# Kernel optimization log

Hardware: AMD Instinct MI355X
Metric: run time of the kernel (lower is better)

The kernel has to match this reference:

```python
import jax, jax.numpy as jnp
import numpy as np

N, CIN, T, V = 32, 64, 256, 25
COUT = 192
K = 3                      # num_subset
INTER = COUT // 4          # coff_embedding = 4 -> 48
MID = COUT // 3            # 64
EPS = 1e-5


def _bn(x, g, b):
    # training-mode BatchNorm2d over (N, T, V) per channel
    m = x.mean(axis=(0, 2, 3), keepdims=True)
    v = x.var(axis=(0, 2, 3), keepdims=True)
    return (x - m) * jax.lax.rsqrt(v + EPS) * g[None, :, None, None] + b[None, :, None, None]


def _conv1x1(x, w, b):
    # w: [O, C]
    return jnp.einsum('oc,nctv->notv', w, x) + b[None, :, None, None]


def _tconv(x, w, b, pad):
    # w: [O, C, k, 1] temporal conv along T
    y = jax.lax.conv_general_dilated(x, w, (1, 1), ((pad, pad), (0, 0)),
                                     dimension_numbers=('NCHW', 'OIHW', 'NCHW'))
    return y + b[None, :, None, None]


def setup_inputs() -> dict:
    key = jax.random.key(0)
    ks = jax.random.split(key, 24)
    r = lambda i, shape, s=0.05: jax.random.normal(ks[i], shape, jnp.float32) * s
    return {
        'x': r(0, (N, CIN, T, V), 1.0),
        'A': jax.random.uniform(ks[1], (K, V, V), jnp.float32),   # fixed adjacency buffer
        'PA': jnp.full((K, V, V), 1e-6, jnp.float32),
        'Wa': r(2, (K, INTER, CIN)), 'ba': jnp.zeros((K, INTER), jnp.float32),
        'Wb': r(3, (K, INTER, CIN)), 'bb': jnp.zeros((K, INTER), jnp.float32),
        'Wd': r(4, (K, COUT, CIN)), 'bd': jnp.zeros((K, COUT), jnp.float32),
        'gcn_bn_g': jnp.ones(COUT, jnp.float32), 'gcn_bn_b': jnp.zeros(COUT, jnp.float32),
        'down_w': r(5, (COUT, CIN)), 'down_b': jnp.zeros(COUT, jnp.float32),
        'down_bn_g': jnp.ones(COUT, jnp.float32), 'down_bn_b': jnp.zeros(COUT, jnp.float32),
        'W11': r(6, (COUT, COUT)), 'b11': jnp.zeros(COUT, jnp.float32),
        'W21': r(7, (COUT, COUT)), 'b21': jnp.zeros(COUT, jnp.float32),
        'W31': r(8, (COUT, COUT)), 'b31': jnp.zeros(COUT, jnp.float32),
        'W12': r(9, (MID, COUT, 1, 1)), 'b12': jnp.zeros(MID, jnp.float32),
        'W22': r(10, (MID, COUT, 3, 1)), 'b22': jnp.zeros(MID, jnp.float32),
        'W32': r(11, (MID, COUT, 7, 1)), 'b32': jnp.zeros(MID, jnp.float32),
        'tcn_bn_g': jnp.ones(COUT, jnp.float32), 'tcn_bn_b': jnp.zeros(COUT, jnp.float32),
        'res_w': r(12, (COUT, CIN)), 'res_b': jnp.zeros(COUT, jnp.float32),
        'res_bn_g': jnp.ones(COUT, jnp.float32), 'res_bn_b': jnp.zeros(COUT, jnp.float32),
    }


def reference(x, A, PA, Wa, ba, Wb, bb, Wd, bd, gcn_bn_g, gcn_bn_b,
              down_w, down_b, down_bn_g, down_bn_b,
              W11, b11, W21, b21, W31, b31, W12, b12, W22, b22, W32, b32,
              tcn_bn_g, tcn_bn_b, res_w, res_b, res_bn_g, res_bn_b):
    n, c, t, v = x.shape
    # ---- unit_gcn (all num_subset branches vectorized over axis k) ----
    fa = jnp.einsum('kic,nctv->nkitv', Wa, x) + ba[None, :, :, None, None]
    fb = jnp.einsum('kic,nctv->nkitv', Wb, x) + bb[None, :, :, None, None]
    A1 = fa.transpose(0, 1, 4, 2, 3).reshape(n, K, v, INTER * t)   # [n,k,V,inter*T]
    A2 = fb.reshape(n, K, INTER * t, v)                            # [n,k,inter*T,V]
    scores = jnp.einsum('nkvd,nkdw->nkvw', A1, A2) / A1.shape[-1]
    att = jax.nn.softmax(scores, axis=-2) + (A + PA)[None]         # softmax over rows (dim -2)
    xv = x.reshape(n, c * t, v)
    z = jnp.einsum('ndv,nkvw->nkdw', xv, att).reshape(n, K, c, t, v)
    y = jnp.einsum('koc,nkctv->notv', Wd, z) + bd.sum(axis=0)[None, :, None, None]
    y = _bn(y, gcn_bn_g, gcn_bn_b)
    y = y + _bn(_conv1x1(x, down_w, down_b), down_bn_g, down_bn_b)
    g = jax.nn.relu(y)
    # ---- unit_tcn_m: three parallel (1x1 conv -> temporal conv) branches ----
    x1 = _tconv(_conv1x1(g, W11, b11), W12, b12, 0)
    x2 = _tconv(_conv1x1(g, W21, b21), W22, b22, 1)
    x3 = _tconv(_conv1x1(g, W31, b31), W32, b32, 3)
    tm = _bn(jnp.concatenate([x1, x2, x3], axis=1), tcn_bn_g, tcn_bn_b)
    # ---- residual: 1x1 unit_tcn on original input ----
    res = _bn(_conv1x1(x, res_w, res_b), res_bn_g, res_bn_b)
    return jax.nn.relu(tm + res)
```

## Files before the change

kernel.cpp:

```cpp
#include <hip/hip_runtime.h>
#include <hip/hip_bf16.h>
#include <cstdint>
#include <cstddef>

#define EPS_  1e-5f
#define NTV_  204800

typedef unsigned short u16;
typedef __attribute__((ext_vector_type(8))) short short8;
typedef __attribute__((ext_vector_type(4))) float f32x4;

__device__ __forceinline__ float bf2f(u16 u) {
  uint32_t x = (uint32_t)u << 16;
  float f;
  __builtin_memcpy(&f, &x, 4);
  return f;
}
__device__ __forceinline__ u16 f2bf(float f) {
  uint32_t x;
  __builtin_memcpy(&x, &f, 4);
  uint32_t r = (x + 0x7FFFu + ((x >> 16) & 1u)) >> 16;
  return (u16)r;
}

__device__ __forceinline__ void gload_lds16(const u16* g, u16* l) {
  __builtin_amdgcn_global_load_lds(
      (const __attribute__((address_space(1))) uint32_t*)g,
      (__attribute__((address_space(3))) uint32_t*)l, 16, 0, 0);
}

__global__ __launch_bounds__(256) void k_cvtw(
    const float* __restrict__ Wa, const float* __restrict__ Wb_,
    const float* __restrict__ dw, const float* __restrict__ rw,
    const float* __restrict__ W11, const float* __restrict__ W21, const float* __restrict__ W31,
    const float* __restrict__ Wd, const float* __restrict__ W12, const float* __restrict__ W22,
    const float* __restrict__ W32, const float* __restrict__ bd,
    const float* __restrict__ ba, const float* __restrict__ bb,
    const float* __restrict__ downbi, const float* __restrict__ resbi,
    const float* __restrict__ b11, const float* __restrict__ b21, const float* __restrict__ b31,
    u16* __restrict__ WB, float* __restrict__ bd2, float* __restrict__ fbias,
    float* __restrict__ cbias)
{
  int i = blockIdx.x * 256 + threadIdx.x;
  if (i < 9216) { WB[i] = f2bf(Wa[i]); return; }
  i -= 9216;
  if (i < 9216) { WB[9216 + i] = f2bf(Wb_[i]); return; }
  i -= 9216;
  if (i < 12288) { WB[18432 + i] = f2bf(dw[i]); return; }
  i -= 12288;
  if (i < 12288) { WB[30720 + i] = f2bf(rw[i]); return; }
  i -= 12288;
  if (i < 36864) { WB[43008 + i] = f2bf(W11[i]); return; }
  i -= 36864;
  if (i < 36864) { WB[79872 + i] = f2bf(W21[i]); return; }
  i -= 36864;
  if (i < 36864) { WB[116736 + i] = f2bf(W31[i]); return; }
  i -= 36864;
  if (i < 36864) {
    const int o = i / 192, r = i % 192, k = r >> 6, c = r & 63;
    WB[153600 + i] = f2bf(Wd[((size_t)(k * 192 + o)) * 64 + c]);
    return;
  }
  i -= 36864;
  if (i < 12288) { WB[190464 + i] = f2bf(W12[i]); return; }
  i -= 12288;
  if (i < 36864) {
    const int tap = i / 12288, q = i % 12288, o = q / 192, c = q % 192;
    WB[202752 + i] = f2bf(W22[((size_t)(o * 192 + c)) * 3 + tap]);
    return;
  }
  i -= 36864;
  if (i < 86016) {
    const int tap = i / 12288, q = i % 12288, o = q / 192, c = q % 192;
    WB[239616 + i] = f2bf(W32[((size_t)(o * 192 + c)) * 7 + tap]);
    return;
  }
  i -= 86016;
  if (i < 192) { bd2[i] = bd[i] + bd[192 + i] + bd[384 + i]; return; }
  i -= 192;
  if (i < 288) { fbias[i] = (i < 144) ? ba[i] : bb[i - 144]; return; }
  i -= 288;
  if (i < 960) {
    const int g = i / 192, o = i % 192;
    float v;
    if (g == 0) v = downbi[o];
    else if (g == 1) v = resbi[o];
    else if (g == 2) v = b11[o];
    else if (g == 3) v = b21[o];
    else v = b31[o];
    cbias[i] = v;
  }
}

__global__ __launch_bounds__(256) void k_xpose(const float* __restrict__ x, u16* __restrict__ xb)
{
  __shared__ u16 xt[256][72];
  const int bx = blockIdx.x;
  const int n = bx / 25, s0 = (bx % 25) * 256;
  const int tid = threadIdx.x;
  for (int l = tid; l < 64 * 64; l += 256) {
    const int c = l >> 6, q = l & 63;
    float4 v = *(const float4*)&x[((size_t)n * 64 + c) * 6400 + s0 + q * 4];
    xt[q * 4 + 0][c] = f2bf(v.x);
    xt[q * 4 + 1][c] = f2bf(v.y);
    xt[q * 4 + 2][c] = f2bf(v.z);
    xt[q * 4 + 3][c] = f2bf(v.w);
  }
  __syncthreads();
  for (int l = tid; l < 256 * 8; l += 256) {
    const int row = l >> 3, seg = l & 7;
    const int s_old = s0 + row;
    const int dv = s_old % 25, dt = s_old / 25;
    *(uint4*)&xb[((size_t)n * 6400 + dv * 256 + dt) * 64 + seg * 8] = *(const uint4*)&xt[row][seg * 8];
  }
}

template<int C, int NP, bool STATS>
__global__ __launch_bounds__(192) void k_conv5(
    const u16* __restrict__ in, const u16* __restrict__ Wb,
    const float* __restrict__ bias,
    u16* __restrict__ out0, u16* __restrict__ out1, u16* __restrict__ out2,
    float* __restrict__ stSum, float* __restrict__ stSq)
{
  constexpr int CS = C / 8;
  constexpr int CH = C / 32;
  constexpr int SB = 128 * CS;
  __shared__ u16 Bt[128 * C];
  __shared__ u16 Ep[3][16 * 72];

  const int bx = blockIdx.x;
  const int nb = bx / 50;
  const int sb = (bx % 50) * 128;
  const int tid = threadIdx.x;
  const int w = tid >> 6, lane = tid & 63;
  const int lr = lane & 15, lg = lane >> 4;

  for (int base = 0; base < SB; base += 192) {
    const int slot = base + tid;
    if ((SB % 192 == 0) || slot < SB) {
      const int r = slot / CS, q = slot % CS;
      gload_lds16(&in[((size_t)nb * 6400 + sb + r) * C + ((q ^ (r & 7)) << 3)],
                  &Bt[(size_t)(base + w * 64) * 8]);
    }
  }
  __syncthreads();

  u16* sc = Ep[w];
  const int o_w = w * 64;
  const int s0 = lane >> 3, seg = lane & 7;

  for (int p = 0; p < NP; ++p) {
    u16* outp = (p == 0) ? out0 : ((p == 1) ? out1 : out2);
    const u16* Ap = Wb + (size_t)p * 192 * C;
    short8 af[4][CH];
#pragma unroll
    for (int mi = 0; mi < 4; ++mi)
#pragma unroll
      for (int j = 0; j < CH; ++j)
        af[mi][j] = *(const short8*)&Ap[((size_t)(o_w + mi * 16 + lr)) * C + j * 32 + lg * 8];
    float4 bv[4];
#pragma unroll
    for (int mi = 0; mi < 4; ++mi)
      bv[mi] = *(const float4*)&bias[p * 192 + o_w + mi * 16 + lg * 4];
    float ssum[4][4] = {}, ssq[4][4] = {};

#pragma unroll
    for (int t = 0; t < 8; ++t) {
      f32x4 acc[4];
#pragma unroll
      for (int mi = 0; mi < 4; ++mi) {
        acc[mi][0] = 0.f; acc[mi][1] = 0.f; acc[mi][2] = 0.f; acc[mi][3] = 0.f;
      }
      const int rr = t * 16 + lr;
#pragma unroll
      for (int j = 0; j < CH; ++j) {
        short8 bf = *(const short8*)&Bt[((size_t)rr * CS + ((j * 4 + lg) ^ (rr & 7))) * 8];
#pragma unroll
        for (int mi = 0; mi < 4; ++mi)
          acc[mi] = __builtin_amdgcn_mfma_f32_16x16x32_bf16(af[mi][j], bf, acc[mi], 0, 0, 0);
      }
#pragma unroll
      for (int mi = 0; mi < 4; ++mi)
#pragma unroll
        for (int r = 0; r < 4; ++r) {
          float vv = acc[mi][r] + ((const float*)&bv[mi])[r];
          if (STATS) { ssum[mi][r] += vv; ssq[mi][r] += vv * vv; }
          sc[lr * 72 + mi * 16 + lg * 4 + r] = f2bf(vv);
        }
#pragma unroll
      for (int pass = 0; pass < 2; ++pass) {
        const int s = pass * 8 + s0;
        uint4 val = *(const uint4*)&sc[s * 72 + seg * 8];
        *(uint4*)&outp[((size_t)nb * 6400 + sb + t * 16 + s) * 192 + o_w + seg * 8] = val;
      }
    }

    if (STATS) {
#pragma unroll
      for (int mi = 0; mi < 4; ++mi)
#pragma unroll
        for (int r = 0; r < 4; ++r) {
          float ss = ssum[mi][r], sq = ssq[mi][r];
#pragma unroll
          for (int m = 1; m < 16; m <<= 1) { ss += __shfl_xor(ss, m); sq += __shfl_xor(sq, m); }
          if (lr == 0) {
            const int og = p * 192 + o_w + mi * 16 + lg * 4 + r;
            const int slot = bx & 15;
            atomicAdd(&stSum[og * 16 + slot], ss);
            atomicAdd(&stSq[og * 16 + slot], sq);
          }
        }
    }
  }
}

__global__ __launch_bounds__(256) void k_tconv7(
    const u16* __restrict__ b1, const u16* __restrict__ b2, const u16* __restrict__ b3,
    const u16* __restrict__ WB,
    const float* __restrict__ bias12, const float* __restrict__ bias22, const float* __restrict__ bias32,
    u16* __restrict__ out, float* __restrict__ stSum, float* __restrict__ stSq,
    const u16* __restrict__ zp)
{
  constexpr int C = 192, CS = 24, CH = 6;
  constexpr int BR = 70;
  __shared__ u16 Bt[BR * C];
  __shared__ u16 Ep[64][200];

  const int bx = blockIdx.x;
  const int nb = bx / 100;
  const int sb = (bx % 100) * 64;
  const int tbase = sb & 255;
  const int tid = threadIdx.x;
  const int w = tid >> 6, lane = tid & 63;
  const int lr = lane & 15, lg = lane >> 4;

  for (int br = 0; br < 3; ++br) {
    const u16* in = (br == 0) ? b1 : ((br == 1) ? b2 : b3);
    const float* bias = (br == 0) ? bias12 : ((br == 1) ? bias22 : bias32);
    const int KT = (br == 0) ? 1 : ((br == 1) ? 3 : 7);
    const u16* Wp = WB + ((br == 0) ? 190464 : ((br == 1) ? 202752 : 239616));

    if (br) __syncthreads();
    constexpr int SB = BR * CS;
    for (int base = 0; base < SB; base += 256) {
      const int slot = base + tid;
      if (slot < SB) {
        const int r = slot / CS, q = slot % CS;
        const int t = tbase - 3 + r;
        const u16* src = ((unsigned)t < 256u)
            ? &in[((size_t)nb * 6400 + sb - 3 + r) * C + ((q ^ (r & 7)) << 3)]
            : zp;
        gload_lds16(src, &Bt[(size_t)(base + w * 64) * 8]);
      }
    }
    __syncthreads();

    f32x4 acc[4];
#pragma unroll
    for (int t = 0; t < 4; ++t) {
      acc[t][0] = 0.f; acc[t][1] = 0.f; acc[t][2] = 0.f; acc[t][3] = 0.f;
    }
    const int hofs = 3 - KT / 2;
    for (int tap = 0; tap < KT; ++tap) {
      short8 af[CH];
#pragma unroll
      for (int j = 0; j < CH; ++j)
        af[j] = *(const short8*)&Wp[((size_t)(tap * 64 + w * 16 + lr)) * C + j * 32 + lg * 8];
#pragma unroll
      for (int t = 0; t < 4; ++t) {
        const int rr = t * 16 + lr + hofs + tap;
#pragma unroll
        for (int j = 0; j < CH; ++j) {
          short8 bf = *(const short8*)&Bt[((size_t)rr * CS + ((j * 4 + lg) ^ (rr & 7))) * 8];
          acc[t] = __builtin_amdgcn_mfma_f32_16x16x32_bf16(af[j], bf, acc[t], 0, 0, 0);
        }
      }
    }

    const float4 bv4 = *(const float4*)&bias[w * 16 + lg * 4];
    float ssum[4] = {}, ssq[4] = {};
#pragma unroll
    for (int t = 0; t < 4; ++t) {
      union { uint2 u; u16 s[4]; } pk;
#pragma unroll
      for (int r = 0; r < 4; ++r) {
        float vv = acc[t][r] + ((const float*)&bv4)[r];
        ssum[r] += vv; ssq[r] += vv * vv;
        pk.s[r] = f2bf(vv);
      }
      *(uint2*)&Ep[t * 16 + lr][br * 64 + w * 16 + lg * 4] = pk.u;
    }
#pragma unroll
    for (int r = 0; r < 4; ++r) {
      float ss = ssum[r], sq = ssq[r];
#pragma unroll
      for (int m = 1; m < 16; m <<= 1) { ss += __shfl_xor(ss, m); sq += __shfl_xor(sq, m); }
      if (lr == 0) {
        const int og = br * 64 + w * 16 + lg * 4 + r;
        const int slot = bx & 15;
        atomicAdd(&stSum[og * 16 + slot], ss);
        atomicAdd(&stSq[og * 16 + slot], sq);
      }
    }
  }
  __syncthreads();

#pragma unroll
  for (int pass = 0; pass < 6; ++pass) {
    const int idx = pass * 256 + tid;
    const int row = idx / 24, ch = idx % 24;
    *(uint4*)&out[((size_t)nb * 6400 + sb + row) * 192 + ch * 8] = *(const uint4*)&Ep[row][ch * 8];
  }
}

__global__ __launch_bounds__(256) void k_gemm_cf(
    const u16* __restrict__ in, const u16* __restrict__ Wb,
    const float* __restrict__ bias, u16* __restrict__ out)
{
  __shared__ u16 Bt[128 * 64];
  __shared__ u16 At[288 * 64];
  __shared__ u16 SC[48 * 136];

  const int bx = blockIdx.x;
  const int nb = bx / 50;
  const int sb = (bx % 50) * 128;
  const int v = sb >> 8, tbase = sb & 255;
  const int tid = threadIdx.x;
  const int w = tid >> 6, lane = tid & 63;
  const int lr = lane & 15, lg = lane >> 4;
  const int s_w = w * 32;

  for (int base = 0; base < 1024; base += 256) {
    const int slot = base + tid;
    const int r = slot >> 3, q = slot & 7;
    gload_lds16(&in[((size_t)nb * 6400 + v * 256 + tbase + r) * 64 + ((q ^ (r & 7)) << 3)],
                &Bt[(size_t)(base + w * 64) * 8]);
  }
  for (int base = 0; base < 2304; base += 256) {
    const int slot = base + tid;
    const int r = slot >> 3, q = slot & 7;
    gload_lds16(&Wb[(size_t)r * 64 + ((q ^ (r & 7)) << 3)],
                &At[(size_t)(base + w * 64) * 8]);
  }
  __syncthreads();

  for (int p = 0; p < 6; ++p) {
    f32x4 acc[3][2];
#pragma unroll
    for (int mi = 0; mi < 3; ++mi)
#pragma unroll
      for (int ni = 0; ni < 2; ++ni) {
        acc[mi][ni][0] = 0.f; acc[mi][ni][1] = 0.f; acc[mi][ni][2] = 0.f; acc[mi][ni][3] = 0.f;
      }
#pragma unroll
    for (int ch = 0; ch < 2; ++ch) {
      const int j = ch * 4 + lg;
      short8 af[3], bf[2];
#pragma unroll
      for (int mi = 0; mi < 3; ++mi) {
        const int r = p * 48 + mi * 16 + lr;
        af[mi] = *(const short8*)&At[((size_t)r * 8 + (j ^ (r & 7))) * 8];
      }
#pragma unroll
      for (int ni = 0; ni < 2; ++ni) {
        const int r = s_w + ni * 16 + lr;
        bf[ni] = *(const short8*)&Bt[((size_t)r * 8 + (j ^ (r & 7))) * 8];
      }
#pragma unroll
      for (int mi = 0; mi < 3; ++mi)
#pragma unroll
        for (int ni = 0; ni < 2; ++ni)
          acc[mi][ni] = __builtin_amdgcn_mfma_f32_16x16x32_bf16(af[mi], bf[ni], acc[mi][ni], 0, 0, 0);
    }
#pragma unroll
    for (int mi = 0; mi < 3; ++mi)
#pragma unroll
      for (int r = 0; r < 4; ++r) {
        const float bv = bias[p * 48 + mi * 16 + lg * 4 + r];
#pragma unroll
        for (int ni = 0; ni < 2; ++ni) acc[mi][ni][r] += bv;
      }
    __syncthreads();
#pragma unroll
    for (int mi = 0; mi < 3; ++mi)
#pragma unroll
      for (int ni = 0; ni < 2; ++ni)
#pragma unroll
        for (int r = 0; r < 4; ++r)
          SC[(mi * 16 + lg * 4 + r) * 136 + s_w + ni * 16 + lr] = f2bf(acc[mi][ni][r]);
    __syncthreads();
#pragma unroll
    for (int it = 0; it < 3; ++it) {
      const int row = it * 16 + (tid >> 4), chunk = tid & 15;
      *(uint4*)&out[((size_t)nb * 288 + p * 48 + row) * 6400 + sb + chunk * 8] =
          *(const uint4*)&SC[row * 136 + chunk * 8];
    }
  }
}

__device__ __forceinline__ float dot4(uint2 a, uint2 b) {
  return bf2f((u16)(a.x & 0xffff)) * bf2f((u16)(b.x & 0xffff)) +
         bf2f((u16)(a.x >> 16))    * bf2f((u16)(b.x >> 16)) +
         bf2f((u16)(a.y & 0xffff)) * bf2f((u16)(b.y & 0xffff)) +
         bf2f((u16)(a.y >> 16))    * bf2f((u16)(b.y >> 16));
}

__global__ __launch_bounds__(256) void k_scores_part(
    const u16* __restrict__ fab, float* __restrict__ part)
{
  const int nk = blockIdx.x;
  const int seg = blockIdx.y;
  const int n = nk / 3, k = nk % 3;
  __shared__ u16 sa[12800], sb[12800];
  const int tid = threadIdx.x;
  const u16* fap = fab + ((size_t)(n * 288 + k * 48 + seg * 2)) * 6400;
  const u16* fbp = fab + ((size_t)(n * 288 + 144 + k * 48 + seg * 2)) * 6400;
  for (int l = tid; l < 1600; l += 256) {
    ((uint4*)sa)[l] = ((const uint4*)fap)[l];
    ((uint4*)sb)[l] = ((const uint4*)fbp)[l];
  }
  __syncthreads();

  const int l0 = tid, l1 = tid + 256, l2 = tid + 512;
  const bool ok2 = (l2 < 625);
  const int v0 = l0 / 25, w0 = l0 % 25;
  const int v1 = l1 / 25, w1 = l1 % 25;
  const int v2 = ok2 ? l2 / 25 : 0, w2 = ok2 ? l2 % 25 : 0;
  float a0 = 0.f, a1 = 0.f, a2 = 0.f;
  const int rot = ((tid & 63) * 4) & 255;

#pragma unroll
  for (int ch = 0; ch < 2; ++ch) {
    const u16* pa = sa + ch * 6400;
    const u16* pb = sb + ch * 6400;
    for (int it = 0; it < 64; ++it) {
      const int t = (it * 4 + rot) & 255;
      a0 += dot4(*(const uint2*)&pa[v0 * 256 + t], *(const uint2*)&pb[w0 * 256 + t]);
      a1 += dot4(*(const uint2*)&pa[v1 * 256 + t], *(const uint2*)&pb[w1 * 256 + t]);
      if (ok2)
        a2 += dot4(*(const uint2*)&pa[v2 * 256 + t], *(const uint2*)&pb[w2 * 256 + t]);
    }
  }
  float* po = part + ((size_t)nk * 24 + seg) * 640;
  po[l0] = a0;
  po[l1] = a1;
  if (ok2) po[l2] = a2;
}

__global__ __launch_bounds__(256) void k_softmax(
    const float* __restrict__ part, const float* __restrict__ A,
    const float* __restrict__ PA, float* __restrict__ att)
{
  const int nk = blockIdx.x;
  const int n = nk / 3, k = nk % 3;
  __shared__ float sc[640];
  const int tid = threadIdx.x;
  const float* pb = part + (size_t)nk * 24 * 640;
  for (int l = tid; l < 625; l += 256) {
    float s = 0.f;
#pragma unroll
    for (int seg = 0; seg < 24; ++seg) s += pb[seg * 640 + l];
    sc[l] = s;
  }
  __syncthreads();
  if (tid < 25) {
    const int w = tid;
    const float scale = 1.f / 12288.f;
    float m = -1e30f;
    for (int v = 0; v < 25; ++v) m = fmaxf(m, sc[v * 25 + w]);
    m *= scale;
    float e[25], sum = 0.f;
#pragma unroll
    for (int v = 0; v < 25; ++v) { e[v] = __expf(sc[v * 25 + w] * scale - m); sum += e[v]; }
    const float inv = 1.f / sum;
    const float* Ak = A + k * 625;
    const float* Pk = PA + k * 625;
    float* ao = att + ((size_t)n * 3 + k) * 625;
#pragma unroll
    for (int v = 0; v < 25; ++v) ao[v * 25 + w] = e[v] * inv + Ak[v * 25 + w] + Pk[v * 25 + w];
  }
}

__global__ __launch_bounds__(256) void k_z(
    const u16* __restrict__ xb, const float* __restrict__ att, u16* __restrict__ z)
{
  __shared__ float attl[1950];
  __shared__ u16 xt[12800];
  const int bx = blockIdx.x;
  const int n = bx >> 5, tb = (bx & 31) * 8;
  const int tid = threadIdx.x;

  for (int l = tid; l < 1875; l += 256) {
    const int k = l / 625, vw = l % 625, v = vw / 25, w = vw % 25;
    attl[(k * 25 + v) * 26 + w] = att[((size_t)n * 3 + k) * 625 + vw];
  }
  for (int l = tid; l < 200 * 8; l += 256) {
    const int j = l >> 3, seg = l & 7;
    const int vv = j >> 3, tl = j & 7;
    *(uint4*)&xt[j * 64 + seg * 8] =
        *(const uint4*)&xb[((size_t)n * 6400 + vv * 256 + tb + tl) * 64 + seg * 8];
  }
  __syncthreads();

  for (int it = 0; it < 19; ++it) {
    const int l = tid + it * 256;
    if (l >= 4800) break;
    const int hi = l >> 6, lo = l & 63;
    const int k = hi / 25, w = hi % 25;
    const int tl = lo >> 3, c0 = (lo & 7) * 8;
    float accv[8] = {};
    for (int v = 0; v < 25; ++v) {
      const float aw = attl[(k * 25 + v) * 26 + w];
      union { uint4 u; u16 s[8]; } xv;
      xv.u = *(const uint4*)&xt[(v * 8 + tl) * 64 + c0];
#pragma unroll
      for (int jj = 0; jj < 8; ++jj) accv[jj] += aw * bf2f(xv.s[jj]);
    }
    union { uint4 u; u16 s[8]; } ov;
#pragma unroll
    for (int jj = 0; jj < 8; ++jj) ov.s[jj] = f2bf(accv[jj]);
    *(uint4*)&z[((size_t)n * 6400 + w * 256 + tb + tl) * 192 + k * 64 + c0] = ov.u;
  }
}

__global__ void k_bnparams(const float* __restrict__ sSum, const float* __restrict__ sSq,
                           const float* __restrict__ gamma, const float* __restrict__ beta,
                           float* __restrict__ a, float* __restrict__ c, int O)
{
  const int o = threadIdx.x + blockIdx.x * blockDim.x;
  if (o >= O) return;
  float sum = 0.f, sq = 0.f;
#pragma unroll
  for (int s = 0; s < 16; ++s) { sum += sSum[o * 16 + s]; sq += sSq[o * 16 + s]; }
  const float mean = sum * (1.f / NTV_);
  const float var = sq * (1.f / NTV_) - mean * mean;
  const float inv = rsqrtf(var + EPS_);
  const float av = gamma[o] * inv;
  a[o] = av;
  c[o] = beta[o] - av * mean;
}

__global__ __launch_bounds__(256) void k_g2(
    const u16* __restrict__ ypre, const u16* __restrict__ down,
    const float* __restrict__ ga, const float* __restrict__ gc,
    const float* __restrict__ da, const float* __restrict__ dc,
    u16* __restrict__ g)
{
  __shared__ float pA1[192], pC1[192], pA2[192], pC2[192];
  const int tid = threadIdx.x;
  if (tid < 192) { pA1[tid] = ga[tid]; pC1[tid] = gc[tid]; pA2[tid] = da[tid]; pC2[tid] = dc[tid]; }
  __syncthreads();
  for (size_t i8 = (size_t)blockIdx.x * 256 + tid; i8 < 4915200; i8 += (size_t)gridDim.x * 256) {
    const int c0 = (int)(i8 % 24) * 8;
    union { uint4 u; u16 s[8]; } yv, dv, ov;
    yv.u = *(const uint4*)&ypre[i8 * 8];
    dv.u = *(const uint4*)&down[i8 * 8];
#pragma unroll
    for (int j = 0; j < 8; ++j) {
      const int c = c0 + j;
      ov.s[j] = f2bf(fmaxf(pA1[c] * bf2f(yv.s[j]) + pC1[c] + pA2[c] * bf2f(dv.s[j]) + pC2[c], 0.f));
    }
    *(uint4*)&g[i8 * 8] = ov.u;
  }
}

__global__ __launch_bounds__(256) void k_out(
    const u16* __restrict__ tm, const u16* __restrict__ resp,
    const float* __restrict__ ta, const float* __restrict__ tc,
    const float* __restrict__ ra, const float* __restrict__ rc,
    float* __restrict__ out)
{
  __shared__ u16 L[100][200];
  __shared__ float pA1[192], pC1[192], pA2[192], pC2[192];
  const int bx = blockIdx.x;
  const int n = bx >> 6, t0 = (bx & 63) * 4;
  const int tid = threadIdx.x;
  if (tid < 192) { pA1[tid] = ta[tid]; pC1[tid] = tc[tid]; pA2[tid] = ra[tid]; pC2[tid] = rc[tid]; }
  __syncthreads();
  for (int l = tid; l < 2400; l += 256) {
    const int row = l / 24, ch = l % 24;
    const int v = row >> 2, tl = row & 3;
    const size_t src = ((size_t)n * 6400 + v * 256 + t0 + tl) * 192 + ch * 8;
    union { uint4 u; u16 s[8]; } tv, rv;
    tv.u = *(const uint4*)&tm[src];
    rv.u = *(const uint4*)&resp[src];
#pragma unroll
    for (int j = 0; j < 8; ++j) {
      const int c = ch * 8 + j;
      L[row][c] = f2bf(fmaxf(pA1[c] * bf2f(tv.s[j]) + pC1[c] + pA2[c] * bf2f(rv.s[j]) + pC2[c], 0.f));
    }
  }
  __syncthreads();
  for (int j = tid; j < 192 * 25; j += 256) {
    const int o = j / 25, q = j % 25;
    float4 f4;
#pragma unroll
    for (int e = 0; e < 4; ++e) {
      const int idx = q * 4 + e;
      const int tl = idx / 25, v = idx % 25;
      ((float*)&f4)[e] = bf2f(L[v * 4 + tl][o]);
    }
    *(float4*)&out[((size_t)n * 192 + o) * 6400 + t0 * 25 + q * 4] = f4;
  }
}

extern "C" void kernel_launch(void* const* d_in, const int* in_sizes, int n_in,
                              void* d_out, int out_size, void* d_ws, size_t ws_size,
                              hipStream_t stream)
{
  const float* x      = (const float*)d_in[0];
  const float* A      = (const float*)d_in[1];
  const float* PA     = (const float*)d_in[2];
  const float* Wa     = (const float*)d_in[3];
  const float* ba     = (const float*)d_in[4];
  const float* Wb     = (const float*)d_in[5];
  const float* bb     = (const float*)d_in[6];
  const float* Wd     = (const float*)d_in[7];
  const float* bd     = (const float*)d_in[8];
  const float* gcng   = (const float*)d_in[9];
  const float* gcnb   = (const float*)d_in[10];
  const float* downw  = (const float*)d_in[11];
  const float* downbi = (const float*)d_in[12];
  const float* downg  = (const float*)d_in[13];
  const float* downb  = (const float*)d_in[14];
  const float* W11    = (const float*)d_in[15];
  const float* b11    = (const float*)d_in[16];
  const float* W21    = (const float*)d_in[17];
  const float* b21    = (const float*)d_in[18];
  const float* W31    = (const float*)d_in[19];
  const float* b31    = (const float*)d_in[20];
  const float* W12    = (const float*)d_in[21];
  const float* b12    = (const float*)d_in[22];
  const float* W22    = (const float*)d_in[23];
  const float* b22    = (const float*)d_in[24];
  const float* W32    = (const float*)d_in[25];
  const float* b32    = (const float*)d_in[26];
  const float* tcng   = (const float*)d_in[27];
  const float* tcnb   = (const float*)d_in[28];
  const float* resw   = (const float*)d_in[29];
  const float* resbi  = (const float*)d_in[30];
  const float* resg   = (const float*)d_in[31];
  const float* resb   = (const float*)d_in[32];
  (void)in_sizes; (void)n_in; (void)out_size; (void)ws_size;

  u16* ob = (u16*)d_out;
  u16* fab   = ob;
  u16* xb    = ob + 58982400;
  float* att = (float*)(ob + 72089600);
  float* part  = (float*)(ob + 72584768);
  float* fbias = (float*)(ob + 75533888);
  u16* btmp2 = ob;
  u16* btmp3 = ob + 39321600;

  char* ws = (char*)d_ws;
  const size_t SLOT = 78643200;
  u16* z     = (u16*)(ws);
  u16* g     = (u16*)(ws);
  u16* ypre  = (u16*)(ws + SLOT);
  u16* btmp1 = (u16*)(ws + SLOT);
  u16* down  = (u16*)(ws + 2 * SLOT);
  u16* tm    = (u16*)(ws + 2 * SLOT);
  u16* resp  = (u16*)(ws + 3 * SLOT);
  char* sm   = ws + 4 * SLOT;
  float* bnp   = (float*)(sm);
  u16*   zp    = (u16*)(sm + 8192);
  u16*   WB    = (u16*)(sm + 8704);
  float* bd2   = (float*)(sm + 660224);
  float* cbias = (float*)(sm + 661248);
  float* slots = (float*)(sm + 665600);
  float* gcnSum = slots;           float* gcnSq = slots + 3072;
  float* dwnSum = slots + 6144;    float* resSum = slots + 9216;
  float* dwnSq  = slots + 12288;   float* resSq  = slots + 15360;
  float* tmSum  = slots + 18432;   float* tmSq   = slots + 21504;
  float* gcnA = bnp;          float* gcnC = bnp + 192;
  float* dwnA = bnp + 384;    float* dwnC = bnp + 576;
  float* resA = bnp + 768;    float* resC = bnp + 960;
  float* tmA  = bnp + 1152;   float* tmC  = bnp + 1344;

  hipMemsetAsync(slots, 0, 24576 * 4, stream);
  hipMemsetAsync(zp, 0, 256, stream);

  const dim3 blk(256);
  const dim3 blk3(192);

  k_cvtw<<<dim3(1278), blk, 0, stream>>>(Wa, Wb, downw, resw, W11, W21, W31,
                                         Wd, W12, W22, W32, bd, ba, bb,
                                         downbi, resbi, b11, b21, b31,
                                         WB, bd2, fbias, cbias);
  k_xpose<<<dim3(800), blk, 0, stream>>>(x, xb);

  k_gemm_cf<<<dim3(1600), blk, 0, stream>>>(xb, WB, fbias, fab);
  k_scores_part<<<dim3(96, 24), blk, 0, stream>>>(fab, part);
  k_softmax<<<dim3(96), blk, 0, stream>>>(part, A, PA, att);
  k_z<<<dim3(1024), blk, 0, stream>>>(xb, att, z);
  k_conv5<192, 1, true><<<dim3(1600), blk3, 0, stream>>>(
      z, WB + 153600, bd2, ypre, ypre, ypre, gcnSum, gcnSq);
  k_conv5<64, 2, true><<<dim3(1600), blk3, 0, stream>>>(
      xb, WB + 18432, cbias, down, resp, resp, dwnSum, dwnSq);
  k_bnparams<<<dim3(1), dim3(192), 0, stream>>>(gcnSum, gcnSq, gcng, gcnb, gcnA, gcnC, 192);
  k_bnparams<<<dim3(1), dim3(192), 0, stream>>>(dwnSum, dwnSq, downg, downb, dwnA, dwnC, 192);
  k_bnparams<<<dim3(1), dim3(192), 0, stream>>>(resSum, resSq, resg, resb, resA, resC, 192);
  k_g2<<<dim3(2048), blk, 0, stream>>>(ypre, down, gcnA, gcnC, dwnA, dwnC, g);

  k_conv5<192, 3, false><<<dim3(1600), blk3, 0, stream>>>(
      g, WB + 43008, cbias + 384, btmp1, btmp2, btmp3, nullptr, nullptr);
  k_tconv7<<<dim3(3200), blk, 0, stream>>>(
      btmp1, btmp2, btmp3, WB, b12, b22, b32, tm, tmSum, tmSq, zp);
  k_bnparams<<<dim3(1), dim3(192), 0, stream>>>(tmSum, tmSq, tcng, tcnb, tmA, tmC, 192);

  k_out<<<dim3(2048), blk, 0, stream>>>(tm, resp, tmA, tmC, resA, resC, (float*)d_out);
}
```

Baseline: 946.8 us.

## Fold 1x1 convs into temporal conv weights, eliminating intermediate branch tensors

Each branch's 1x1 conv (W11/W21/W31) is algebraically composed into the following temporal conv weights per tap, precomputed by a small kernel along with per-tap bias contributions. The temporal conv now reads the shared activation g once into LDS instead of three separate branch intermediates. This removes a 192-channel, three-output GEMM pass and the write and read of three large intermediate tensors. In exchange, bias at sequence edges needs per-tap correction for zero padding, and the combined weights are rounded to bf16 after composition, which changes numerics slightly.

```diff
diff --git a/kernel.cpp b/kernel.cpp
--- a/kernel.cpp
+++ b/kernel.cpp
@@ -32,12 +32,9 @@
 __global__ __launch_bounds__(256) void k_cvtw(
     const float* __restrict__ Wa, const float* __restrict__ Wb_,
     const float* __restrict__ dw, const float* __restrict__ rw,
-    const float* __restrict__ W11, const float* __restrict__ W21, const float* __restrict__ W31,
-    const float* __restrict__ Wd, const float* __restrict__ W12, const float* __restrict__ W22,
-    const float* __restrict__ W32, const float* __restrict__ bd,
+    const float* __restrict__ Wd, const float* __restrict__ bd,
     const float* __restrict__ ba, const float* __restrict__ bb,
     const float* __restrict__ downbi, const float* __restrict__ resbi,
-    const float* __restrict__ b11, const float* __restrict__ b21, const float* __restrict__ b31,
     u16* __restrict__ WB, float* __restrict__ bd2, float* __restrict__ fbias,
     float* __restrict__ cbias)
 {
@@ -50,46 +47,62 @@
   i -= 12288;
   if (i < 12288) { WB[30720 + i] = f2bf(rw[i]); return; }
   i -= 12288;
-  if (i < 36864) { WB[43008 + i] = f2bf(W11[i]); return; }
-  i -= 36864;
-  if (i < 36864) { WB[79872 + i] = f2bf(W21[i]); return; }
-  i -= 36864;
-  if (i < 36864) { WB[116736 + i] = f2bf(W31[i]); return; }
-  i -= 36864;
   if (i < 36864) {
     const int o = i / 192, r = i % 192, k = r >> 6, c = r & 63;
-    WB[153600 + i] = f2bf(Wd[((size_t)(k * 192 + o)) * 64 + c]);
+    WB[43008 + i] = f2bf(Wd[((size_t)(k * 192 + o)) * 64 + c]);
     return;
   }
   i -= 36864;
-  if (i < 12288) { WB[190464 + i] = f2bf(W12[i]); return; }
-  i -= 12288;
-  if (i < 36864) {
-    const int tap = i / 12288, q = i % 12288, o = q / 192, c = q % 192;
-    WB[202752 + i] = f2bf(W22[((size_t)(o * 192 + c)) * 3 + tap]);
-    return;
-  }
-  i -= 36864;
-  if (i < 86016) {
-    const int tap = i / 12288, q = i % 12288, o = q / 192, c = q % 192;
-    WB[239616 + i] = f2bf(W32[((size_t)(o * 192 + c)) * 7 + tap]);
-    return;
-  }
-  i -= 86016;
   if (i < 192) { bd2[i] = bd[i] + bd[192 + i] + bd[384 + i]; return; }
   i -= 192;
   if (i < 288) { fbias[i] = (i < 144) ? ba[i] : bb[i - 144]; return; }
   i -= 288;
-  if (i < 960) {
+  if (i < 384) {
     const int g = i / 192, o = i % 192;
-    float v;
-    if (g == 0) v = downbi[o];
-    else if (g == 1) v = resbi[o];
-    else if (g == 2) v = b11[o];
-    else if (g == 3) v = b21[o];
-    else v = b31[o];
-    cbias[i] = v;
-  }
+    cbias[i] = (g == 0) ? downbi[o] : resbi[o];
+  }
+}
+
+__global__ __launch_bounds__(256) void k_wcomp(
+    const float* __restrict__ W11, const float* __restrict__ W21, const float* __restrict__ W31,
+    const float* __restrict__ W12, const float* __restrict__ W22, const float* __restrict__ W32,
+    const float* __restrict__ b11, const float* __restrict__ b21, const float* __restrict__ b31,
+    u16* __restrict__ WC, float* __restrict__ btap)
+{
+  const int tapg = blockIdx.x;
+  const float* W1; const float* W2; const float* b1; int tapl, KT;
+  if (tapg == 0)      { W1 = W11; W2 = W12; b1 = b11; tapl = 0;        KT = 1; }
+  else if (tapg < 4)  { W1 = W21; W2 = W22; b1 = b21; tapl = tapg - 1; KT = 3; }
+  else                { W1 = W31; W2 = W32; b1 = b31; tapl = tapg - 4; KT = 7; }
+  const int tid = threadIdx.x;
+  for (int i = 0; i < 48; ++i) {
+    const int idx = tid + i * 256;
+    const int o = idx / 192, c = idx % 192;
+    float s = 0.f;
+    for (int m = 0; m < 192; ++m)
+      s += W2[((size_t)o * 192 + m) * KT + tapl] * W1[(size_t)m * 192 + c];
+    WC[(size_t)tapg * 12288 + idx] = f2bf(s);
+  }
+  if (tid < 64) {
+    float s = 0.f;
+    for (int m = 0; m < 192; ++m)
+      s += W2[((size_t)tid * 192 + m) * KT + tapl] * b1[m];
+    btap[tapg * 64 + tid] = s;
+  }
+}
+
+__global__ void k_bfull(const float* __restrict__ btap,
+                        const float* __restrict__ b12, const float* __restrict__ b22,
+                        const float* __restrict__ b32, float* __restrict__ bfull)
+{
+  const int tid = threadIdx.x;
+  if (tid >= 192) return;
+  const int br = tid / 64, o = tid % 64;
+  float s = (br == 0) ? b12[o] : ((br == 1) ? b22[o] : b32[o]);
+  const int t0 = (br == 0) ? 0 : ((br == 1) ? 1 : 4);
+  const int kt = (br == 0) ? 1 : ((br == 1) ? 3 : 7);
+  for (int tap = 0; tap < kt; ++tap) s += btap[(t0 + tap) * 64 + o];
+  bfull[tid] = s;
 }
 
 __global__ __launch_bounds__(256) void k_xpose(const float* __restrict__ x, u16* __restrict__ xb)
@@ -214,16 +227,14 @@
   }
 }
 
-__global__ __launch_bounds__(256) void k_tconv7(
-    const u16* __restrict__ b1, const u16* __restrict__ b2, const u16* __restrict__ b3,
-    const u16* __restrict__ WB,
-    const float* __restrict__ bias12, const float* __restrict__ bias22, const float* __restrict__ bias32,
+__global__ __launch_bounds__(256) void k_tconv9(
+    const u16* __restrict__ g, const u16* __restrict__ WC,
+    const float* __restrict__ bfull, const float* __restrict__ btap,
     u16* __restrict__ out, float* __restrict__ stSum, float* __restrict__ stSq,
     const u16* __restrict__ zp)
 {
-  constexpr int C = 192, CS = 24, CH = 6;
-  constexpr int BR = 70;
-  __shared__ u16 Bt[BR * C];
+  constexpr int CS = 24, CH = 6;
+  __shared__ u16 Bt[70 * 192];
   __shared__ u16 Ep[64][200];
 
   const int bx = blockIdx.x;
@@ -234,26 +245,26 @@
   const int w = tid >> 6, lane = tid & 63;
   const int lr = lane & 15, lg = lane >> 4;
 
+  constexpr int SB = 70 * CS;
+  for (int base = 0; base < SB; base += 256) {
+    const int slot = base + tid;
+    if (slot < SB) {
+      const int r = slot / CS, q = slot % CS;
+      const int t = tbase - 3 + r;
+      const u16* src = ((unsigned)t < 256u)
+          ? &g[((size_t)nb * 6400 + sb - 3 + r) * 192 + ((q ^ (r & 7)) << 3)]
+          : zp;
+      gload_lds16(src, &Bt[(size_t)(base + w * 64) * 8]);
+    }
+  }
+  __syncthreads();
+
+  const bool edge = (tbase == 0) || (tbase == 192);
+
   for (int br = 0; br < 3; ++br) {
-    const u16* in = (br == 0) ? b1 : ((br == 1) ? b2 : b3);
-    const float* bias = (br == 0) ? bias12 : ((br == 1) ? bias22 : bias32);
     const int KT = (br == 0) ? 1 : ((br == 1) ? 3 : 7);
-    const u16* Wp = WB + ((br == 0) ? 190464 : ((br == 1) ? 202752 : 239616));
-
-    if (br) __syncthreads();
-    constexpr int SB = BR * CS;
-    for (int base = 0; base < SB; base += 256) {
-      const int slot = base + tid;
-      if (slot < SB) {
-        const int r = slot / CS, q = slot % CS;
-        const int t = tbase - 3 + r;
-        const u16* src = ((unsigned)t < 256u)
-            ? &in[((size_t)nb * 6400 + sb - 3 + r) * C + ((q ^ (r & 7)) << 3)]
-            : zp;
-        gload_lds16(src, &Bt[(size_t)(base + w * 64) * 8]);
-      }
-    }
-    __syncthreads();
+    const int tb0 = (br == 0) ? 0 : ((br == 1) ? 1 : 4);
+    const u16* Wp = WC + (size_t)tb0 * 12288;
 
     f32x4 acc[4];
 #pragma unroll
@@ -265,7 +276,7 @@
       short8 af[CH];
 #pragma unroll
       for (int j = 0; j < CH; ++j)
-        af[j] = *(const short8*)&Wp[((size_t)(tap * 64 + w * 16 + lr)) * C + j * 32 + lg * 8];
+        af[j] = *(const short8*)&Wp[((size_t)(tap * 64 + w * 16 + lr)) * 192 + j * 32 + lg * 8];
 #pragma unroll
       for (int t = 0; t < 4; ++t) {
         const int rr = t * 16 + lr + hofs + tap;
@@ -277,14 +288,29 @@
       }
     }
 
-    const float4 bv4 = *(const float4*)&bias[w * 16 + lg * 4];
+    float bb[4];
+    {
+      const float4 bv = *(const float4*)&bfull[br * 64 + w * 16 + lg * 4];
+      bb[0] = bv.x; bb[1] = bv.y; bb[2] = bv.z; bb[3] = bv.w;
+    }
     float ssum[4] = {}, ssq[4] = {};
 #pragma unroll
     for (int t = 0; t < 4; ++t) {
+      float b4[4] = {bb[0], bb[1], bb[2], bb[3]};
+      if (KT > 1 && edge) {
+        const int trow = tbase + t * 16 + lr;
+        for (int tap = 0; tap < KT; ++tap) {
+          const int dt = tap - KT / 2;
+          if ((unsigned)(trow + dt) >= 256u) {
+            const float4 bv = *(const float4*)&btap[(tb0 + tap) * 64 + w * 16 + lg * 4];
+            b4[0] -= bv.x; b4[1] -= bv.y; b4[2] -= bv.z; b4[3] -= bv.w;
+          }
+        }
+      }
       union { uint2 u; u16 s[4]; } pk;
 #pragma unroll
       for (int r = 0; r < 4; ++r) {
-        float vv = acc[t][r] + ((const float*)&bv4)[r];
+        float vv = acc[t][r] + b4[r];
         ssum[r] += vv; ssq[r] += vv * vv;
         pk.s[r] = f2bf(vv);
       }
@@ -649,15 +675,15 @@
   float* att = (float*)(ob + 72089600);
   float* part  = (float*)(ob + 72584768);
   float* fbias = (float*)(ob + 75533888);
-  u16* btmp2 = ob;
-  u16* btmp3 = ob + 39321600;
+  u16*   WC    = ob + 75534464;
+  float* btap  = (float*)(ob + 75669760);
+  float* bfull = (float*)(ob + 75671296);
 
   char* ws = (char*)d_ws;
   const size_t SLOT = 78643200;
   u16* z     = (u16*)(ws);
   u16* g     = (u16*)(ws);
   u16* ypre  = (u16*)(ws + SLOT);
-  u16* btmp1 = (u16*)(ws + SLOT);
   u16* down  = (u16*)(ws + 2 * SLOT);
   u16* tm    = (u16*)(ws + 2 * SLOT);
   u16* resp  = (u16*)(ws + 3 * SLOT);
@@ -683,10 +709,11 @@
   const dim3 blk(256);
   const dim3 blk3(192);
 
-  k_cvtw<<<dim3(1278), blk, 0, stream>>>(Wa, Wb, downw, resw, W11, W21, W31,
-                                         Wd, W12, W22, W32, bd, ba, bb,
-                                         downbi, resbi, b11, b21, b31,
-                                         WB, bd2, fbias, cbias);
+  k_cvtw<<<dim3(316), blk, 0, stream>>>(Wa, Wb, downw, resw, Wd, bd, ba, bb,
+                                        downbi, resbi, WB, bd2, fbias, cbias);
+  k_wcomp<<<dim3(11), blk, 0, stream>>>(W11, W21, W31, W12, W22, W32,
+                                        b11, b21, b31, WC, btap);
+  k_bfull<<<dim3(1), dim3(192), 0, stream>>>(btap, b12, b22, b32, bfull);
   k_xpose<<<dim3(800), blk, 0, stream>>>(x, xb);
 
   k_gemm_cf<<<dim3(1600), blk, 0, stream>>>(xb, WB, fbias, fab);
@@ -694,7 +721,7 @@
   k_softmax<<<dim3(96), blk, 0, stream>>>(part, A, PA, att);
   k_z<<<dim3(1024), blk, 0, stream>>>(xb, att, z);
   k_conv5<192, 1, true><<<dim3(1600), blk3, 0, stream>>>(
-      z, WB + 153600, bd2, ypre, ypre, ypre, gcnSum, gcnSq);
+      z, WB + 43008, bd2, ypre, ypre, ypre, gcnSum, gcnSq);
   k_conv5<64, 2, true><<<dim3(1600), blk3, 0, stream>>>(
       xb, WB + 18432, cbias, down, resp, resp, dwnSum, dwnSq);
   k_bnparams<<<dim3(1), dim3(192), 0, stream>>>(gcnSum, gcnSq, gcng, gcnb, gcnA, gcnC, 192);
@@ -702,10 +729,8 @@
   k_bnparams<<<dim3(1), dim3(192), 0, stream>>>(resSum, resSq, resg, resb, resA, resC, 192);
   k_g2<<<dim3(2048), blk, 0, stream>>>(ypre, down, gcnA, gcnC, dwnA, dwnC, g);
 
-  k_conv5<192, 3, false><<<dim3(1600), blk3, 0, stream>>>(
-      g, WB + 43008, cbias + 384, btmp1, btmp2, btmp3, nullptr, nullptr);
-  k_tconv7<<<dim3(3200), blk, 0, stream>>>(
-      btmp1, btmp2, btmp3, WB, b12, b22, b32, tm, tmSum, tmSq, zp);
+  k_tconv9<<<dim3(3200), blk, 0, stream>>>(
+      g, WC, bfull, btap, tm, tmSum, tmSq, zp);
   k_bnparams<<<dim3(1), dim3(192), 0, stream>>>(tmSum, tmSq, tcng, tcnb, tmA, tmC, 192);
 
   k_out<<<dim3(2048), blk, 0, stream>>>(tm, resp, tmA, tmC, resA, resC, (float*)d_out);
```

New measurement: 1.495 ms. 1.58x slower.
